# Kernel tuning notes

Hardware: AMD Instinct MI355X
Metric: run time of the kernel (lower is better)

Reference implementation:

```python
import jax, jax.numpy as jnp
import numpy as np
jax.config.update("jax_enable_x64", True)

B, N, FEAT_DIM, OUT_DIM = 16, 10000, 256, 256
CH = [3, 64, 64, 64, 128, FEAT_DIM]  # ptlk PointNet_features MLP widths (scale=1)
BN_EPS = 1e-5
L2_EPS = 1e-12


def setup_inputs() -> dict:
    key = jax.random.key(0)
    ks = jax.random.split(key, 2 * len(CH) + 4)
    inp = {"points": jax.random.normal(ks[0], (B, N, 3), dtype=jnp.float32)}
    for i in range(5):
        cin, cout = CH[i], CH[i + 1]
        inp[f"W{i}"] = jax.random.normal(ks[1 + 2 * i], (cout, cin), dtype=jnp.float32) / np.sqrt(cin).astype(np.float32)
        inp[f"g{i}"] = jnp.ones((cout,), jnp.float32)
        inp[f"b{i}"] = jnp.zeros((cout,), jnp.float32)
    inp["Wfc"] = jax.random.normal(ks[-2], (OUT_DIM, FEAT_DIM * FEAT_DIM), dtype=jnp.float32) / np.sqrt(FEAT_DIM * FEAT_DIM).astype(np.float32)
    inp["bfc"] = jnp.zeros((OUT_DIM,), jnp.float32)
    return inp


def _bn_relu(y, g, b):
    # training-mode BatchNorm1d over (batch, points) per channel; y: [B,C,N]
    mu = jnp.mean(y, axis=(0, 2), keepdims=True)
    var = jnp.var(y, axis=(0, 2), keepdims=True)
    y = (y - mu) * jax.lax.rsqrt(var + BN_EPS)
    return jax.nn.relu(y * g[None, :, None] + b[None, :, None])


def reference(points, W0, g0, b0, W1, g1, b1, W2, g2, b2, W3, g3, b3, W4, g4, b4, Wfc, bfc):
    x = jnp.transpose(points, (0, 2, 1))  # [B,3,N]
    for W, g, b in ((W0, g0, b0), (W1, g1, b1), (W2, g2, b2), (W3, g3, b3), (W4, g4, b4)):
        x = jnp.einsum('oc,bcn->bon', W, x)  # 1x1 conv1d
        x = _bn_relu(x, g, b)
    f = jnp.transpose(x, (0, 2, 1))  # [B,N,D] per-point features
    # so_cov: global mean over all B*N points (as in the original), then per-batch covariance
    mean = jnp.mean(f.reshape(-1, FEAT_DIM), axis=0)  # [D]
    fc = f - mean
    cov = jnp.einsum('bnd,bne->bde', fc, fc) / np.float32(N)  # [B,D,D]
    # matrix square-root via fp64 SVD (torch: x.double(); u s v = svd; u diag(s^0.5) v^T)
    u, s, vh = jnp.linalg.svd(cov.astype(jnp.float64), full_matrices=False)
    sqrt_cov = (u * jnp.sqrt(s)[:, None, :]) @ vh  # [B,D,D]
    v = sqrt_cov.reshape(f.shape[0], FEAT_DIM * FEAT_DIM).astype(jnp.float32)
    out = v @ Wfc.T + bfc  # [B,OUT_DIM]
    norm = jnp.maximum(jnp.linalg.norm(out, axis=-1, keepdims=True), L2_EPS)
    return out / norm
```

## Files before the change

### kernel.cpp

```cpp
#include <hip/hip_runtime.h>
#include <cmath>

constexpr int NB   = 16;
constexpr int NPTS = 10000;
constexpr int NBN  = NB * NPTS;
constexpr int NS_ITERS = 18;
constexpr int COV_CHUNKS = 20;
constexpr int CHUNK_PTS  = 500;
constexpr int COV_KK     = 16;

typedef _Float16 f16x8 __attribute__((ext_vector_type(8)));
typedef float  f32x4  __attribute__((ext_vector_type(4)));
typedef unsigned short ushort4v __attribute__((ext_vector_type(4)));
typedef unsigned short ushort8v __attribute__((ext_vector_type(8)));

__global__ __launch_bounds__(256) void conv0_ker(const float* __restrict__ pts,
                                                 const float* __restrict__ W,
                                                 float* __restrict__ y) {
    int g = blockIdx.x * 256 + threadIdx.x;
    int b = g / NPTS;
    int n = g - b * NPTS;
    float p0 = pts[3 * (size_t)g + 0];
    float p1 = pts[3 * (size_t)g + 1];
    float p2 = pts[3 * (size_t)g + 2];
    float* yp = y + ((size_t)b * 64) * NPTS + n;
    for (int o = 0; o < 64; ++o) {
        float v = W[3 * o] * p0 + W[3 * o + 1] * p1 + W[3 * o + 2] * p2;
        yp[(size_t)o * NPTS] = v;
    }
}

__device__ __forceinline__ unsigned short f2h(float f) {
    return __builtin_bit_cast(unsigned short, (_Float16)f);
}
__device__ __forceinline__ float hres(float f) {
    return f - (float)(_Float16)f;
}
__device__ __forceinline__ int swzu(int us) {
    return us ^ (((us >> 7) & 3) << 4);
}
__device__ __forceinline__ int swz8(int byteoff) {
    return byteoff ^ (((byteoff >> 8) & 3) << 5);
}

template <int CIN, int COUT, int OTILE>
__global__ __launch_bounds__(256) void conv_mfma(const float* __restrict__ xin,
                                                 const float* __restrict__ ss,
                                                 const float* __restrict__ W,
                                                 float* __restrict__ y,
                                                 float* __restrict__ stats) {
    constexpr int OT = OTILE / 16;
    constexpr int WM = 4;
    constexpr int WN = (OTILE == 128) ? 4 : 2;
    constexpr int NCW = (OTILE == 128) ? 2 : 4;
    __shared__ unsigned short Xp[2][8 * 512];
    __shared__ unsigned short Wp[2][OT * 512];

    const int tid  = threadIdx.x;
    const int lane = tid & 63;
    const int w    = tid >> 6;
    const int wr   = (OTILE == 128) ? (w & 1) : 0;
    const int wc   = (OTILE == 128) ? (w >> 1) : w;

    const int nb = blockIdx.x * 128;
    const int ob = blockIdx.y * OTILE;
    const int b  = blockIdx.z;

    f32x4 acc[WM][WN];
#pragma unroll
    for (int m = 0; m < WM; ++m)
#pragma unroll
        for (int n = 0; n < WN; ++n) acc[m][n] = (f32x4){0.f, 0.f, 0.f, 0.f};

    const int xn = tid & 127;
    const int th = tid >> 7;
    const bool nok = (nb + xn) < NPTS;

#pragma unroll 1
    for (int kc = 0; kc < CIN; kc += 32) {
        __syncthreads();
#pragma unroll
        for (int i = 0; i < OTILE / 32; ++i) {
            int l = i * 256 + tid;
            int o = l >> 3, k4 = (l & 7) << 2;
            float4 v = *(const float4*)(W + (size_t)(ob + o) * CIN + kc + k4);
            ushort4v h4, l4;
            h4[0] = f2h(v.x); l4[0] = f2h(hres(v.x));
            h4[1] = f2h(v.y); l4[1] = f2h(hres(v.y));
            h4[2] = f2h(v.z); l4[2] = f2h(hres(v.z));
            h4[3] = f2h(v.w); l4[3] = f2h(hres(v.w));
            int us = swzu((o >> 4) * 512 + ((k4 >> 3) * 16 + (o & 15)) * 8 + (k4 & 7));
            *(ushort4v*)&Wp[0][us] = h4;
            *(ushort4v*)&Wp[1][us] = l4;
        }
#pragma unroll
        for (int qq = 0; qq < 2; ++qq) {
            int q = th * 2 + qq;
            const float* xb = xin + ((size_t)(b * CIN + kc + q * 8)) * NPTS + nb + xn;
            float f[8];
#pragma unroll
            for (int j = 0; j < 8; ++j) {
                float v = nok ? xb[(size_t)j * NPTS] : 0.f;
                int c = kc + q * 8 + j;
                f[j] = fmaxf(fmaf(v, ss[c], ss[256 + c]), 0.f);
            }
            ushort8v h8, l8;
#pragma unroll
            for (int j = 0; j < 8; ++j) {
                h8[j] = f2h(f[j]);
                l8[j] = f2h(hres(f[j]));
            }
            int us = swzu((xn >> 4) * 512 + (q * 16 + (xn & 15)) * 8);
            *(ushort8v*)&Xp[0][us] = h8;
            *(ushort8v*)&Xp[1][us] = l8;
        }
        __syncthreads();

        f16x8 ah[WM], al[WM], bh[WN], bl[WN];
#pragma unroll
        for (int m = 0; m < WM; ++m) {
            int us = swzu((wr * WM + m) * 512 + lane * 8);
            ah[m] = *(const f16x8*)&Wp[0][us];
            al[m] = *(const f16x8*)&Wp[1][us];
        }
#pragma unroll
        for (int n = 0; n < WN; ++n) {
            int us = swzu((wc * WN + n) * 512 + lane * 8);
            bh[n] = *(const f16x8*)&Xp[0][us];
            bl[n] = *(const f16x8*)&Xp[1][us];
        }
#pragma unroll
        for (int m = 0; m < WM; ++m)
#pragma unroll
            for (int n = 0; n < WN; ++n) {
                acc[m][n] = __builtin_amdgcn_mfma_f32_16x16x32_f16(ah[m], bh[n], acc[m][n], 0, 0, 0);
                acc[m][n] = __builtin_amdgcn_mfma_f32_16x16x32_f16(ah[m], bl[n], acc[m][n], 0, 0, 0);
                acc[m][n] = __builtin_amdgcn_mfma_f32_16x16x32_f16(al[m], bh[n], acc[m][n], 0, 0, 0);
            }
    }

    const int ro = (lane >> 4) * 4;
    const int co = lane & 15;
#pragma unroll
    for (int m = 0; m < WM; ++m) {
        int o = ob + wr * (WM * 16) + m * 16 + ro;
#pragma unroll
        for (int n = 0; n < WN; ++n) {
            int col = nb + wc * (WN * 16) + n * 16 + co;
            if (col < NPTS) {
                float* yp = y + ((size_t)(b * COUT + o)) * NPTS + col;
#pragma unroll
                for (int r = 0; r < 4; ++r)
                    yp[(size_t)r * NPTS] = acc[m][n][r];
            }
        }
    }

    __syncthreads();
    float* sbuf = (float*)&Xp[0][0];
    float* qbuf = sbuf + NCW * OTILE;
#pragma unroll
    for (int m = 0; m < WM; ++m)
#pragma unroll
        for (int r = 0; r < 4; ++r) {
            float s = 0.f, q = 0.f;
#pragma unroll
            for (int n = 0; n < WN; ++n) {
                int col = nb + wc * (WN * 16) + n * 16 + co;
                float v = acc[m][n][r];
                if (col < NPTS) { s += v; q = fmaf(v, v, q); }
            }
            s += __shfl_xor(s, 1); q += __shfl_xor(q, 1);
            s += __shfl_xor(s, 2); q += __shfl_xor(q, 2);
            s += __shfl_xor(s, 4); q += __shfl_xor(q, 4);
            s += __shfl_xor(s, 8); q += __shfl_xor(q, 8);
            if (co == 0) {
                int rowl = wr * (WM * 16) + m * 16 + ro + r;
                sbuf[wc * OTILE + rowl] = s;
                qbuf[wc * OTILE + rowl] = q;
            }
        }
    __syncthreads();
    if (tid < OTILE) {
        float s = 0.f, q = 0.f;
#pragma unroll
        for (int j = 0; j < NCW; ++j) {
            s += sbuf[j * OTILE + tid];
            q += qbuf[j * OTILE + tid];
        }
        atomicAdd(&stats[ob + tid], s);
        atomicAdd(&stats[COUT + ob + tid], q);
    }
}

__global__ void chan_stats(const float* __restrict__ y, int C, float* __restrict__ stats) {
    int c = blockIdx.x, b = blockIdx.y, t = threadIdx.x;
    const float* p = y + ((size_t)(b * C + c)) * NPTS;
    float s = 0.f, q = 0.f;
    for (int n = t; n < NPTS; n += 256) {
        float v = p[n];
        s += v;
        q = fmaf(v, v, q);
    }
    for (int off = 32; off; off >>= 1) {
        s += __shfl_down(s, off);
        q += __shfl_down(q, off);
    }
    __shared__ float ls[4], lq[4];
    if ((t & 63) == 0) { ls[t >> 6] = s; lq[t >> 6] = q; }
    __syncthreads();
    if (t == 0) {
        atomicAdd(&stats[c],     ls[0] + ls[1] + ls[2] + ls[3]);
        atomicAdd(&stats[C + c], lq[0] + lq[1] + lq[2] + lq[3]);
    }
}

__global__ void bn_finalize(const float* __restrict__ stats, const float* __restrict__ g,
                            const float* __restrict__ bi, int C, float* __restrict__ ss) {
    int c = threadIdx.x;
    if (c < C) {
        float mu  = stats[c] * (1.f / NBN);
        float var = stats[C + c] * (1.f / NBN) - mu * mu;
        float r = rsqrtf(var + 1e-5f);
        float s = g[c] * r;
        ss[c] = s;
        ss[256 + c] = bi[c] - mu * s;
    }
}

template <int NPAN>
__device__ __forceinline__ void cov_issue(const float* __restrict__ y4, int b,
                                          int ti, int tj, int chb, int p4,
                                          int n0c, int kk, float4 (&cur)[NPAN][4]) {
    const int nbase = n0c + kk * 32;
#pragma unroll
    for (int p = 0; p < NPAN; ++p) {
        const int pcb = (p ? tj : ti) * 128;
#pragma unroll
        for (int i = 0; i < 4; ++i) {
            const int ch = chb + 32 * i;
            float4 v = make_float4(0.f, 0.f, 0.f, 0.f);
            if (kk * 32 + p4 < CHUNK_PTS)
                v = *(const float4*)(y4 + ((size_t)(b * 256 + pcb + ch)) * NPTS + nbase + p4);
            cur[p][i] = v;
        }
    }
}

template <int NPAN>
__global__ __launch_bounds__(256) void cov_mfma(const float* __restrict__ y4,
                                                const float* __restrict__ ss,
                                                float* __restrict__ covP,
                                                float* __restrict__ fsumb) {
    __shared__ unsigned short pan[NPAN][2][4096];

    const int chunk = blockIdx.x;
    const int tile  = (NPAN == 2) ? 2 : (int)blockIdx.y;
    const int b     = blockIdx.z;
    const int ti = (tile == 1) ? 1 : 0;
    const int tj = (tile == 0) ? 0 : 1;

    const int tid  = threadIdx.x;
    const int lane = tid & 63;
    const int w    = tid >> 6;
    const int wr   = w & 1, wc = w >> 1;
    const int n0c  = chunk * CHUNK_PTS;

    f32x4 acc[4][4];
#pragma unroll
    for (int m = 0; m < 4; ++m)
#pragma unroll
        for (int n = 0; n < 4; ++n) acc[m][n] = (f32x4){0.f, 0.f, 0.f, 0.f};

    const int g   = tid & 7;
    const int chb = tid >> 3;
    const int p4  = g * 4;
    const int q   = p4 >> 3, j0 = p4 & 7;

    float fs[4] = {0.f, 0.f, 0.f, 0.f};
    float4 cur[NPAN][4];

    cov_issue<NPAN>(y4, b, ti, tj, chb, p4, n0c, 0, cur);

#pragma unroll 1
    for (int kk = 0; kk < COV_KK; ++kk) {
        __builtin_amdgcn_sched_barrier(0);
        __builtin_amdgcn_s_barrier();
        __builtin_amdgcn_sched_barrier(0);

        const bool ok = (kk * 32 + p4 < CHUNK_PTS);
#pragma unroll
        for (int p = 0; p < NPAN; ++p) {
            const int pcb = (p ? tj : ti) * 128;
#pragma unroll
            for (int i = 0; i < 4; ++i) {
                const int ch = chb + 32 * i;
                float4 v = cur[p][i];
                if (ok) {
                    float sc = ss[pcb + ch], sh = ss[256 + pcb + ch];
                    v.x = fmaxf(fmaf(v.x, sc, sh), 0.f);
                    v.y = fmaxf(fmaf(v.y, sc, sh), 0.f);
                    v.z = fmaxf(fmaf(v.z, sc, sh), 0.f);
                    v.w = fmaxf(fmaf(v.w, sc, sh), 0.f);
                } else {
                    v = make_float4(0.f, 0.f, 0.f, 0.f);
                }
                if (NPAN == 1) fs[i] += (v.x + v.y) + (v.z + v.w);
                ushort4v h4, l4;
                h4[0] = f2h(v.x); l4[0] = f2h(hres(v.x));
                h4[1] = f2h(v.y); l4[1] = f2h(hres(v.y));
                h4[2] = f2h(v.z); l4[2] = f2h(hres(v.z));
                h4[3] = f2h(v.w); l4[3] = f2h(hres(v.w));
                const int addr = (ch >> 4) * 512 + (q * 16 + (ch & 15)) * 8 + j0;
                const int sa = swz8(addr * 2) >> 1;
                *(ushort4v*)&pan[p][0][sa] = h4;
                *(ushort4v*)&pan[p][1][sa] = l4;
            }
        }
        if (kk + 1 < COV_KK)
            cov_issue<NPAN>(y4, b, ti, tj, chb, p4, n0c, kk + 1, cur);

        asm volatile("s_waitcnt lgkmcnt(0)" ::: "memory");
        __builtin_amdgcn_s_barrier();
        __builtin_amdgcn_sched_barrier(0);

        const unsigned short* Ah = pan[0][0];
        const unsigned short* Al = pan[0][1];
        const unsigned short* Bh = pan[NPAN - 1][0];
        const unsigned short* Bl = pan[NPAN - 1][1];

        f16x8 ah[4], al[4], bh[4], bl[4];
#pragma unroll
        for (int m = 0; m < 4; ++m) {
            int t8 = (wr * 4 + m) * 512 + lane * 8;
            int sa = swz8(t8 * 2) >> 1;
            ah[m] = *(const f16x8*)&Ah[sa];
            al[m] = *(const f16x8*)&Al[sa];
        }
#pragma unroll
        for (int n = 0; n < 4; ++n) {
            int t8 = (wc * 4 + n) * 512 + lane * 8;
            int sa = swz8(t8 * 2) >> 1;
            bh[n] = *(const f16x8*)&Bh[sa];
            bl[n] = *(const f16x8*)&Bl[sa];
        }
#pragma unroll
        for (int m = 0; m < 4; ++m)
#pragma unroll
            for (int n = 0; n < 4; ++n) {
                acc[m][n] = __builtin_amdgcn_mfma_f32_16x16x32_f16(ah[m], bh[n], acc[m][n], 0, 0, 0);
                acc[m][n] = __builtin_amdgcn_mfma_f32_16x16x32_f16(ah[m], bl[n], acc[m][n], 0, 0, 0);
                acc[m][n] = __builtin_amdgcn_mfma_f32_16x16x32_f16(al[m], bh[n], acc[m][n], 0, 0, 0);
            }
    }

    if (NPAN == 1) {
#pragma unroll
        for (int i = 0; i < 4; ++i) {
            float s = fs[i];
            s += __shfl_xor(s, 1);
            s += __shfl_xor(s, 2);
            s += __shfl_xor(s, 4);
            if (g == 0)
                atomicAdd(&fsumb[b * 256 + ti * 128 + chb + 32 * i], s);
        }
    }

    float* outp = covP + (((size_t)(chunk * NB + b) * 3 + tile) << 14);
    const int rowb = wr * 64;
    const int colb = wc * 64;
#pragma unroll
    for (int m = 0; m < 4; ++m)
#pragma unroll
        for (int n = 0; n < 4; ++n)
#pragma unroll
            for (int r = 0; r < 4; ++r) {
                int row = rowb + m * 16 + (lane >> 4) * 4 + r;
                int col = colb + n * 16 + (lane & 15);
                outp[(row << 7) + col] = acc[m][n][r];
            }
}

__global__ void covfin_ker(const float* __restrict__ covP, const float* __restrict__ fsumb,
                           float* __restrict__ Y0, float* __restrict__ trace) {
    int r = blockIdx.x, b = blockIdx.y, c = threadIdx.x;
    float fbr = fsumb[b * 256 + r] * (1.f / NPTS);
    float fbc = fsumb[b * 256 + c] * (1.f / NPTS);
    float mr = 0.f, mc = 0.f;
    for (int q = 0; q < NB; ++q) {
        mr += fsumb[q * 256 + r];
        mc += fsumb[q * 256 + c];
    }
    mr *= (1.f / NBN);
    mc *= (1.f / NBN);
    int tile, rr, cc;
    if (r < 128 && c < 128)        { tile = 0; rr = r;       cc = c; }
    else if (r >= 128 && c >= 128) { tile = 1; rr = r - 128; cc = c - 128; }
    else if (r < 128)              { tile = 2; rr = r;       cc = c - 128; }
    else                           { tile = 2; rr = c;       cc = r - 128; }
    size_t base = (((size_t)b * 3 + tile) << 14) + ((size_t)rr << 7) + cc;
    float m5 = 0.f;
#pragma unroll
    for (int q = 0; q < COV_CHUNKS; ++q)
        m5 += covP[(size_t)q * (NB * 3 * 16384) + base];
    float v = m5 * (1.f / NPTS) - fbr * mc - mr * fbc + mr * mc;
    Y0[((size_t)b << 16) + ((size_t)r << 8) + c] = v;
    if (c == r) atomicAdd(&trace[b], v);
}

__global__ void ns_init(float* __restrict__ Y0, float* __restrict__ Z0,
                        const float* __restrict__ trace) {
    int i = blockIdx.x * 256 + threadIdx.x;
    int b = i >> 16, rc = i & 65535;
    float inv = 1.f / trace[b];
    Y0[i] *= inv;
    Z0[i] = ((rc >> 8) == (rc & 255)) ? 1.f : 0.f;
}

__device__ __forceinline__ void ns_body8(const float* __restrict__ Ab,
                                         const float* __restrict__ Bb,
                                         float* __restrict__ Ob,
                                         float scale, float diag, int tile, int tid,
                                         unsigned short* Ap0, unsigned short* Ap1,
                                         unsigned short* Bp0, unsigned short* Bp1) {
    const int lane = tid & 63;
    const int w    = tid >> 6;
    const int wr   = w & 3;
    const int wc   = w >> 2;
    const int tr = (tile >> 2) * 64, tc = (tile & 3) * 64;

    f32x4 acc[2];
    acc[0] = (f32x4){0.f, 0.f, 0.f, 0.f};
    acc[1] = (f32x4){0.f, 0.f, 0.f, 0.f};

    const int r2   = tid >> 3;
    const int kq8  = tid & 7;
    const int colB = tid & 63;
    const int kB   = tid >> 6;

#pragma unroll 1
    for (int kc = 0; kc < 256; kc += 64) {
        __syncthreads();
        {
            const float* ap = Ab + (size_t)(tr + r2) * 256 + kc + kq8 * 8;
            float av[8];
            *(float4*)&av[0] = *(const float4*)ap;
            *(float4*)&av[4] = *(const float4*)(ap + 4);
            ushort8v h8, l8;
#pragma unroll
            for (int j = 0; j < 8; ++j) { h8[j] = f2h(av[j]); l8[j] = f2h(hres(av[j])); }
            const int ua = ((r2 >> 4) * 2 + (kq8 >> 2)) * 512 + ((kq8 & 3) * 16 + (r2 & 15)) * 8;
            const int sa = swz8(ua * 2) >> 1;
            *(ushort8v*)&Ap0[sa] = h8;
            *(ushort8v*)&Ap1[sa] = l8;
        }
        {
            const float* bp = Bb + (size_t)(kc + kB * 8) * 256 + tc + colB;
            float bv[8];
#pragma unroll
            for (int j = 0; j < 8; ++j) bv[j] = bp[(size_t)j * 256];
            ushort8v h8, l8;
#pragma unroll
            for (int j = 0; j < 8; ++j) { h8[j] = f2h(bv[j]); l8[j] = f2h(hres(bv[j])); }
            const int ub = ((colB >> 4) * 2 + (kB >> 2)) * 512 + ((kB & 3) * 16 + (colB & 15)) * 8;
            const int sb = swz8(ub * 2) >> 1;
            *(ushort8v*)&Bp0[sb] = h8;
            *(ushort8v*)&Bp1[sb] = l8;
        }
        __syncthreads();

#pragma unroll
        for (int kk = 0; kk < 2; ++kk) {
            const int ua = swz8(((wr * 2 + kk) * 512 + lane * 8) * 2) >> 1;
            f16x8 a_h = *(const f16x8*)&Ap0[ua];
            f16x8 a_l = *(const f16x8*)&Ap1[ua];
#pragma unroll
            for (int n = 0; n < 2; ++n) {
                const int ub = swz8((((wc * 2 + n) * 2 + kk) * 512 + lane * 8) * 2) >> 1;
                f16x8 b_h = *(const f16x8*)&Bp0[ub];
                f16x8 b_l = *(const f16x8*)&Bp1[ub];
                acc[n] = __builtin_amdgcn_mfma_f32_16x16x32_f16(a_h, b_h, acc[n], 0, 0, 0);
                acc[n] = __builtin_amdgcn_mfma_f32_16x16x32_f16(a_h, b_l, acc[n], 0, 0, 0);
                acc[n] = __builtin_amdgcn_mfma_f32_16x16x32_f16(a_l, b_h, acc[n], 0, 0, 0);
            }
        }
    }

    const int ro = (lane >> 4) * 4, co = lane & 15;
#pragma unroll
    for (int n = 0; n < 2; ++n) {
        int row = tr + wr * 16 + ro;
        int col = tc + wc * 32 + n * 16 + co;
#pragma unroll
        for (int r = 0; r < 4; ++r) {
            float v = scale * acc[n][r] + (((row + r) == col) ? diag : 0.f);
            Ob[(size_t)(row + r) * 256 + col] = v;
        }
    }
}

__global__ __launch_bounds__(512) void ns_gemm(const float* __restrict__ A,
                                               const float* __restrict__ B,
                                               float* __restrict__ O,
                                               float scale, float diag) {
    __shared__ unsigned short Ap[2][4096], Bp[2][4096];
    const int id  = blockIdx.x;
    const int xcd = id & 7;
    const int k   = id >> 3;
    const int b   = 2 * xcd + (k >> 4);
    const int tile = k & 15;
    size_t off = (size_t)b << 16;
    ns_body8(A + off, B + off, O + off, scale, diag, tile, threadIdx.x,
             Ap[0], Ap[1], Bp[0], Bp[1]);
}

__global__ __launch_bounds__(512) void ns_gemm_pair(const float* __restrict__ Y,
                                                    const float* __restrict__ Mm,
                                                    const float* __restrict__ Z,
                                                    float* __restrict__ Yn,
                                                    float* __restrict__ Zn) {
    __shared__ unsigned short Ap[2][4096], Bp[2][4096];
    const int id  = blockIdx.x;
    const int xcd = id & 7;
    const int k   = id >> 3;
    const int z   = k >> 5;
    const int rem = k & 31;
    const int b   = 2 * xcd + (rem >> 4);
    const int tile = rem & 15;
    size_t off = (size_t)b << 16;
    if (z == 0)
        ns_body8(Y + off, Mm + off, Yn + off, 0.5f, 0.f, tile, threadIdx.x,
                 Ap[0], Ap[1], Bp[0], Bp[1]);
    else
        ns_body8(Mm + off, Z + off, Zn + off, 0.5f, 0.f, tile, threadIdx.x,
                 Ap[0], Ap[1], Bp[0], Bp[1]);
}

__global__ __launch_bounds__(256) void fc_ker(const float* __restrict__ Yf,
                                              const float* __restrict__ trace,
                                              const float* __restrict__ Wfc,
                                              float* __restrict__ outpre) {
    int kc = blockIdx.x;
    int ot = blockIdx.y;
    int t = threadIdx.x;
    __shared__ float Wl[64][129];
    __shared__ float Vl[16][129];
#pragma unroll
    for (int i = 0; i < 32; ++i) {
        int l = i * 256 + t;
        int o = l >> 7, k = l & 127;
        Wl[o][k] = Wfc[(size_t)(ot * 64 + o) * 65536 + kc * 128 + k];
    }
#pragma unroll
    for (int i = 0; i < 8; ++i) {
        int l = i * 256 + t;
        int bb = l >> 7, k = l & 127;
        Vl[bb][k] = sqrtf(trace[bb]) * Yf[((size_t)bb << 16) + kc * 128 + k];
    }
    __syncthreads();
    int ol = t & 63, bg = t >> 6;
    float a0 = 0.f, a1 = 0.f, a2 = 0.f, a3 = 0.f;
    for (int k = 0; k < 128; ++k) {
        float w = Wl[ol][k];
        a0 = fmaf(w, Vl[bg * 4 + 0][k], a0);
        a1 = fmaf(w, Vl[bg * 4 + 1][k], a1);
        a2 = fmaf(w, Vl[bg * 4 + 2][k], a2);
        a3 = fmaf(w, Vl[bg * 4 + 3][k], a3);
    }
    int o = ot * 64 + ol;
    atomicAdd(&outpre[(bg * 4 + 0) * 256 + o], a0);
    atomicAdd(&outpre[(bg * 4 + 1) * 256 + o], a1);
    atomicAdd(&outpre[(bg * 4 + 2) * 256 + o], a2);
    atomicAdd(&outpre[(bg * 4 + 3) * 256 + o], a3);
}

__global__ void norm_ker(const float* __restrict__ outpre, const float* __restrict__ bfc,
                         float* __restrict__ dout) {
    int b = blockIdx.x, t = threadIdx.x;
    float v = outpre[b * 256 + t] + bfc[t];
    float q = v * v;
    for (int off = 32; off; off >>= 1) q += __shfl_xor(q, off);
    __shared__ float lq[4];
    __shared__ float snorm;
    if ((t & 63) == 0) lq[t >> 6] = q;
    __syncthreads();
    if (t == 0) snorm = fmaxf(sqrtf(lq[0] + lq[1] + lq[2] + lq[3]), 1e-12f);
    __syncthreads();
    dout[b * 256 + t] = v / snorm;
}

extern "C" void kernel_launch(void* const* d_in, const int* in_sizes, int n_in,
                              void* d_out, int out_size, void* d_ws, size_t ws_size,
                              hipStream_t stream) {
    (void)in_sizes; (void)n_in; (void)out_size; (void)ws_size;
    const float* pts = (const float*)d_in[0];
    const float* Wm[5]; const float* gm[5]; const float* bm[5];
    for (int i = 0; i < 5; ++i) {
        Wm[i] = (const float*)d_in[1 + 3 * i];
        gm[i] = (const float*)d_in[2 + 3 * i];
        bm[i] = (const float*)d_in[3 + 3 * i];
    }
    const float* Wfc = (const float*)d_in[16];
    const float* bfc = (const float*)d_in[17];

    float* ws     = (float*)d_ws;
    float* stats  = ws;
    float* fsumb  = ws + 2560;
    float* trace  = ws + 6656;
    float* outpre = ws + 6672;
    float* ss     = ws + 10768;
    float* R      = ws + 16384;
    float* P      = R;
    float* Q      = R + (size_t)NB * 256 * NPTS;
    float* covP   = Q;
    float* Y0     = R;
    float* Y1     = Y0 + 1048576;
    float* Z0     = Y1 + 1048576;
    float* Z1     = Z0 + 1048576;
    float* Mb     = Z1 + 1048576;

    hipMemsetAsync(ws, 0, 16384 * sizeof(float), stream);

    conv0_ker<<<dim3(NBN / 256), dim3(256), 0, stream>>>(pts, Wm[0], P);
    chan_stats<<<dim3(64, NB), dim3(256), 0, stream>>>(P, 64, stats);
    bn_finalize<<<dim3(1), dim3(256), 0, stream>>>(stats, gm[0], bm[0], 64, ss);
    conv_mfma<64, 64, 64><<<dim3(79, 1, NB), dim3(256), 0, stream>>>(P, ss, Wm[1], Q, stats + 512);
    bn_finalize<<<dim3(1), dim3(256), 0, stream>>>(stats + 512, gm[1], bm[1], 64, ss + 512);
    conv_mfma<64, 64, 64><<<dim3(79, 1, NB), dim3(256), 0, stream>>>(Q, ss + 512, Wm[2], P, stats + 1024);
    bn_finalize<<<dim3(1), dim3(256), 0, stream>>>(stats + 1024, gm[2], bm[2], 64, ss + 1024);
    conv_mfma<64, 128, 128><<<dim3(79, 1, NB), dim3(256), 0, stream>>>(P, ss + 1024, Wm[3], Q, stats + 1536);
    bn_finalize<<<dim3(1), dim3(256), 0, stream>>>(stats + 1536, gm[3], bm[3], 128, ss + 1536);
    conv_mfma<128, 256, 128><<<dim3(79, 2, NB), dim3(256), 0, stream>>>(Q, ss + 1536, Wm[4], R, stats + 2048);
    bn_finalize<<<dim3(1), dim3(256), 0, stream>>>(stats + 2048, gm[4], bm[4], 256, ss + 2048);

    cov_mfma<1><<<dim3(COV_CHUNKS, 2, NB), dim3(256), 0, stream>>>(R, ss + 2048, covP, fsumb);
    cov_mfma<2><<<dim3(COV_CHUNKS, 1, NB), dim3(256), 0, stream>>>(R, ss + 2048, covP, fsumb);
    covfin_ker<<<dim3(256, NB), dim3(256), 0, stream>>>(covP, fsumb, Y0, trace);
    ns_init<<<dim3(4096), dim3(256), 0, stream>>>(Y0, Z0, trace);

    float* Yc = Y0; float* Zc = Z0; float* Yn = Y1; float* Zn = Z1;
    for (int it = 0; it < NS_ITERS; ++it) {
        ns_gemm<<<dim3(256), dim3(512), 0, stream>>>(Zc, Yc, Mb, -1.f, 3.f);
        ns_gemm_pair<<<dim3(512), dim3(512), 0, stream>>>(Yc, Mb, Zc, Yn, Zn);
        float* ty = Yc; Yc = Yn; Yn = ty;
        float* tz = Zc; Zc = Zn; Zn = tz;
    }

    fc_ker<<<dim3(512, 4), dim3(256), 0, stream>>>(Yc, trace, Wfc, outpre);
    norm_ker<<<dim3(NB), dim3(256), 0, stream>>>(outpre, bfc, (float*)d_out);
}
```

Measured before the change: 844.9 us.

## Merge covariance kernels into one XCD-mapped launch and widen NS k-tile

The two covariance launches (diagonal tiles and off-diagonal tile) become a single kernel of 960 blocks. Each block decodes its chunk, batch and tile from the block id, and blocks sharing a chunk and batch are grouped on the same XCD so the y4 panels they read can be reused in L2, and one launch boundary disappears. Separately, the Newton-Schulz GEMM body now stages 128 k-values per shared-memory pass instead of 64. This halves the number of sync rounds but doubles LDS use per block, which may lower occupancy.

```diff
diff --git a/kernel.cpp b/kernel.cpp
--- a/kernel.cpp
+++ b/kernel.cpp
@@ -248,19 +248,15 @@
 }
 
 template <int NPAN>
-__global__ __launch_bounds__(256) void cov_mfma(const float* __restrict__ y4,
-                                                const float* __restrict__ ss,
-                                                float* __restrict__ covP,
-                                                float* __restrict__ fsumb) {
-    __shared__ unsigned short pan[NPAN][2][4096];
-
-    const int chunk = blockIdx.x;
-    const int tile  = (NPAN == 2) ? 2 : (int)blockIdx.y;
-    const int b     = blockIdx.z;
+__device__ __forceinline__ void cov_body(const float* __restrict__ y4,
+                                         const float* __restrict__ ss,
+                                         float* __restrict__ covP,
+                                         float* __restrict__ fsumb,
+                                         int chunk, int tile, int b, int tid,
+                                         unsigned short (*pan)[2][4096]) {
     const int ti = (tile == 1) ? 1 : 0;
     const int tj = (tile == 0) ? 0 : 1;
 
-    const int tid  = threadIdx.x;
     const int lane = tid & 63;
     const int w    = tid >> 6;
     const int wr   = w & 1, wc = w >> 1;
@@ -381,6 +377,25 @@
             }
 }
 
+__global__ __launch_bounds__(256) void cov_all(const float* __restrict__ y4,
+                                               const float* __restrict__ ss,
+                                               float* __restrict__ covP,
+                                               float* __restrict__ fsumb) {
+    __shared__ unsigned short pan[2][2][4096];
+    const int id  = blockIdx.x;
+    const int xcd = id & 7;
+    const int j   = id >> 3;
+    const int t3  = j % 3;
+    const int tile = (t3 == 0) ? 2 : (t3 - 1);
+    const int g0  = xcd * 40 + j / 3;
+    const int chunk = g0 >> 4;
+    const int b     = g0 & 15;
+    if (tile == 2)
+        cov_body<2>(y4, ss, covP, fsumb, chunk, 2, b, threadIdx.x, pan);
+    else
+        cov_body<1>(y4, ss, covP, fsumb, chunk, tile, b, threadIdx.x, pan);
+}
+
 __global__ void covfin_ker(const float* __restrict__ covP, const float* __restrict__ fsumb,
                            float* __restrict__ Y0, float* __restrict__ trace) {
     int r = blockIdx.x, b = blockIdx.y, c = threadIdx.x;
@@ -439,30 +454,34 @@
     const int kB   = tid >> 6;
 
 #pragma unroll 1
-    for (int kc = 0; kc < 256; kc += 64) {
+    for (int kc = 0; kc < 256; kc += 128) {
         __syncthreads();
-        {
-            const float* ap = Ab + (size_t)(tr + r2) * 256 + kc + kq8 * 8;
+#pragma unroll
+        for (int kb = 0; kb < 2; ++kb) {
+            const int koct = kq8 + kb * 8;
+            const float* ap = Ab + (size_t)(tr + r2) * 256 + kc + koct * 8;
             float av[8];
             *(float4*)&av[0] = *(const float4*)ap;
             *(float4*)&av[4] = *(const float4*)(ap + 4);
             ushort8v h8, l8;
 #pragma unroll
             for (int j = 0; j < 8; ++j) { h8[j] = f2h(av[j]); l8[j] = f2h(hres(av[j])); }
-            const int ua = ((r2 >> 4) * 2 + (kq8 >> 2)) * 512 + ((kq8 & 3) * 16 + (r2 & 15)) * 8;
+            const int ua = ((r2 >> 4) * 4 + (koct >> 2)) * 512 + ((koct & 3) * 16 + (r2 & 15)) * 8;
             const int sa = swz8(ua * 2) >> 1;
             *(ushort8v*)&Ap0[sa] = h8;
             *(ushort8v*)&Ap1[sa] = l8;
         }
-        {
-            const float* bp = Bb + (size_t)(kc + kB * 8) * 256 + tc + colB;
+#pragma unroll
+        for (int kb = 0; kb < 2; ++kb) {
+            const int koct = kB + kb * 8;
+            const float* bp = Bb + (size_t)(kc + koct * 8) * 256 + tc + colB;
             float bv[8];
 #pragma unroll
             for (int j = 0; j < 8; ++j) bv[j] = bp[(size_t)j * 256];
             ushort8v h8, l8;
 #pragma unroll
             for (int j = 0; j < 8; ++j) { h8[j] = f2h(bv[j]); l8[j] = f2h(hres(bv[j])); }
-            const int ub = ((colB >> 4) * 2 + (kB >> 2)) * 512 + ((kB & 3) * 16 + (colB & 15)) * 8;
+            const int ub = ((colB >> 4) * 4 + (koct >> 2)) * 512 + ((koct & 3) * 16 + (colB & 15)) * 8;
             const int sb = swz8(ub * 2) >> 1;
             *(ushort8v*)&Bp0[sb] = h8;
             *(ushort8v*)&Bp1[sb] = l8;
@@ -470,13 +489,13 @@
         __syncthreads();
 
 #pragma unroll
-        for (int kk = 0; kk < 2; ++kk) {
-            const int ua = swz8(((wr * 2 + kk) * 512 + lane * 8) * 2) >> 1;
+        for (int kk = 0; kk < 4; ++kk) {
+            const int ua = swz8(((wr * 4 + kk) * 512 + lane * 8) * 2) >> 1;
             f16x8 a_h = *(const f16x8*)&Ap0[ua];
             f16x8 a_l = *(const f16x8*)&Ap1[ua];
 #pragma unroll
             for (int n = 0; n < 2; ++n) {
-                const int ub = swz8((((wc * 2 + n) * 2 + kk) * 512 + lane * 8) * 2) >> 1;
+                const int ub = swz8((((wc * 2 + n) * 4 + kk) * 512 + lane * 8) * 2) >> 1;
                 f16x8 b_h = *(const f16x8*)&Bp0[ub];
                 f16x8 b_l = *(const f16x8*)&Bp1[ub];
                 acc[n] = __builtin_amdgcn_mfma_f32_16x16x32_f16(a_h, b_h, acc[n], 0, 0, 0);
@@ -503,7 +522,7 @@
                                                const float* __restrict__ B,
                                                float* __restrict__ O,
                                                float scale, float diag) {
-    __shared__ unsigned short Ap[2][4096], Bp[2][4096];
+    __shared__ unsigned short Ap[2][8192], Bp[2][8192];
     const int id  = blockIdx.x;
     const int xcd = id & 7;
     const int k   = id >> 3;
@@ -519,7 +538,7 @@
                                                     const float* __restrict__ Z,
                                                     float* __restrict__ Yn,
                                                     float* __restrict__ Zn) {
-    __shared__ unsigned short Ap[2][4096], Bp[2][4096];
+    __shared__ unsigned short Ap[2][8192], Bp[2][8192];
     const int id  = blockIdx.x;
     const int xcd = id & 7;
     const int k   = id >> 3;
@@ -633,8 +652,7 @@
     conv_mfma<128, 256, 128><<<dim3(79, 2, NB), dim3(256), 0, stream>>>(Q, ss + 1536, Wm[4], R, stats + 2048);
     bn_finalize<<<dim3(1), dim3(256), 0, stream>>>(stats + 2048, gm[4], bm[4], 256, ss + 2048);
 
-    cov_mfma<1><<<dim3(COV_CHUNKS, 2, NB), dim3(256), 0, stream>>>(R, ss + 2048, covP, fsumb);
-    cov_mfma<2><<<dim3(COV_CHUNKS, 1, NB), dim3(256), 0, stream>>>(R, ss + 2048, covP, fsumb);
+    cov_all<<<dim3(960), dim3(256), 0, stream>>>(R, ss + 2048, covP, fsumb);
     covfin_ker<<<dim3(256, NB), dim3(256), 0, stream>>>(covP, fsumb, Y0, trace);
     ns_init<<<dim3(4096), dim3(256), 0, stream>>>(Y0, Z0, trace);
 
```

After: 843.7 us. About the same (-0.1%).
